# Performance work log

Hardware: AMD Instinct MI355X
Metric: run time of the kernel (lower is better)

The kernel has to match this reference:

```python
import jax, jax.numpy as jnp
import numpy as np

EMBED = 8      # == n_qubits, forced by x[:, i, :].view(batch, n_qubits)
FFN = 4096
B, S = 32, 2048


def setup_inputs() -> dict:
    key = jax.random.key(0)
    k_x, k_t, k_w1, k_b1, k_w2, k_b2 = jax.random.split(key, 6)
    x = jax.random.normal(k_x, (B, S, EMBED), dtype=jnp.float32)
    theta = jax.random.normal(k_t, (), dtype=jnp.float32)  # shared trainable RY angle
    # torch.nn.Linear-style init bounds
    lim1 = 1.0 / np.sqrt(EMBED)
    lim2 = 1.0 / np.sqrt(FFN)
    W1 = jax.random.uniform(k_w1, (FFN, EMBED), jnp.float32, -lim1, lim1)
    b1 = jax.random.uniform(k_b1, (FFN,), jnp.float32, -lim1, lim1)
    W2 = jax.random.uniform(k_w2, (EMBED, FFN), jnp.float32, -lim2, lim2)
    b2 = jax.random.uniform(k_b2, (EMBED,), jnp.float32, -lim2, lim2)
    return {"x": x, "theta": theta, "W1": W1, "b1": b1, "W2": W2, "b2": b2}


def reference(x, theta, W1, b1, W2, b2):
    # Quantum circuit, solved analytically (product state, single-qubit gates):
    # |0> --RX(x_i)--RY(theta)--> <Z_i> = cos(theta) * cos(x_i)
    # This fuses the original per-token Python loop into one elementwise op.
    q = jnp.cos(theta) * jnp.cos(x)                 # [B, S, 8]
    # dropout is identity in eval mode
    h = jax.nn.relu(jnp.einsum('bsk,fk->bsf', q, W1) + b1)   # [B, S, FFN]
    out = jnp.einsum('bsf,ef->bse', h, W2) + b2              # [B, S, 8]
    return out
```

## Files before the change

### kernel.cpp

```cpp
#include <hip/hip_runtime.h>
#include <math.h>

#define FFN_DIM 4096
#define NCHUNK  128

typedef _Float16 f16x8 __attribute__((ext_vector_type(8)));
typedef __fp16   h16x2 __attribute__((ext_vector_type(2)));
typedef float    f32x16 __attribute__((ext_vector_type(16)));
typedef float    f32x4  __attribute__((ext_vector_type(4)));

__global__ void build_frags_kernel(const float* __restrict__ w1,
                                   const float* __restrict__ b1,
                                   const float* __restrict__ w2,
                                   _Float16* __restrict__ w1f,
                                   _Float16* __restrict__ w2f) {
    int i = blockIdx.x * 256 + threadIdx.x;
    if (i < NCHUNK * 64 * 8) {
        int j    = i & 7;
        int lane = (i >> 3) & 63;
        int cc   = i >> 9;
        _Float16 v;
        if (lane < 32) v = (_Float16)w1[(cc * 32 + lane) * 8 + j];
        else           v = (j == 0) ? (_Float16)b1[cc * 32 + (lane & 31)]
                                    : (_Float16)0.0f;
        w1f[i] = v;
    }
    if (i < NCHUNK * 2 * 16 * 8) {
        int j  = i & 7;
        int ci = (i >> 3) & 15;
        int c  = (i >> 7) & 1;
        int cc = i >> 8;
        int g = ci >> 3, e = ci & 7;
        int k = 8 * g + j;
        int fl = (k & 3) + 8 * ((k >> 2) & 1) + 4 * (k >> 3);
        int f = 32 * cc + 16 * c + fl;
        w2f[i] = (_Float16)w2[e * FFN_DIM + f];
    }
}

__global__ __launch_bounds__(256, 2) void ffq_mfma_kernel(
    const float* __restrict__ x,
    const float* __restrict__ theta,
    const _Float16* __restrict__ w1f,
    const _Float16* __restrict__ w2f,
    const float* __restrict__ b2,
    float* __restrict__ out,
    int n_tok)
{
    __shared__ float part[4][4][64][4];

    const int tid  = threadIdx.x;
    const int lane = tid & 63;
    const int wave = tid >> 6;
    const int l31  = lane & 31;
    const int g    = lane >> 5;

    const int tb = blockIdx.x * 128;
    const float cth = cosf(theta[0]);

    f16x8 bq0 = {}, bq1 = {}, bq2 = {}, bq3 = {};
    if (g == 0) {
#define LOAD_BQ(BQ, TOFF)                                                  \
        {                                                                  \
            int t_ = tb + (TOFF) + l31;                                    \
            int r_ = t_ < n_tok ? t_ : (n_tok - 1);                        \
            const f32x4* xp_ = (const f32x4*)(x + (size_t)r_ * 8);         \
            f32x4 u_ = xp_[0], v_ = xp_[1];                                \
            BQ[0] = (_Float16)(cth * cosf(u_.x));                          \
            BQ[1] = (_Float16)(cth * cosf(u_.y));                          \
            BQ[2] = (_Float16)(cth * cosf(u_.z));                          \
            BQ[3] = (_Float16)(cth * cosf(u_.w));                          \
            BQ[4] = (_Float16)(cth * cosf(v_.x));                          \
            BQ[5] = (_Float16)(cth * cosf(v_.y));                          \
            BQ[6] = (_Float16)(cth * cosf(v_.z));                          \
            BQ[7] = (_Float16)(cth * cosf(v_.w));                          \
        }
        LOAD_BQ(bq0, 0)
        LOAD_BQ(bq1, 32)
        LOAD_BQ(bq2, 64)
        LOAD_BQ(bq3, 96)
#undef LOAD_BQ
    } else {
        bq0[0] = (_Float16)1.0f;
        bq1[0] = (_Float16)1.0f;
        bq2[0] = (_Float16)1.0f;
        bq3[0] = (_Float16)1.0f;
    }

    f32x16 acc0 = {}, acc1 = {}, acc2 = {}, acc3 = {};
    const f32x16 zero16 = {};

    const int ci = g * 8 + (l31 & 7);
    const _Float16* a1p = w1f + (size_t)lane * 8;
    const _Float16* a2p = w2f + (size_t)ci * 8;

    union U8 { f16x8 v; h16x2 p[4]; };
    const h16x2 hz = {(__fp16)0.0f, (__fp16)0.0f};

    const int c0 = wave * (NCHUNK / 4);
    const int c1 = c0 + (NCHUNK / 4);

    f16x8 A1  = *(const f16x8*)(a1p + (size_t)c0 * 512);
    f16x8 A2a = *(const f16x8*)(a2p + (size_t)c0 * 256);
    f16x8 A2b = *(const f16x8*)(a2p + (size_t)c0 * 256 + 128);

    for (int cc = c0; cc < c1; ++cc) {
        f16x8 nA1 = A1, nA2a = A2a, nA2b = A2b;
        if (cc + 1 < c1) {
            nA1  = *(const f16x8*)(a1p + (size_t)(cc + 1) * 512);
            nA2a = *(const f16x8*)(a2p + (size_t)(cc + 1) * 256);
            nA2b = *(const f16x8*)(a2p + (size_t)(cc + 1) * 256 + 128);
        }

        f32x16 dA = __builtin_amdgcn_mfma_f32_32x32x16_f16(A1, bq0, zero16, 0, 0, 0);
        f32x16 dB = __builtin_amdgcn_mfma_f32_32x32x16_f16(A1, bq1, zero16, 0, 0, 0);
        f32x16 dC = __builtin_amdgcn_mfma_f32_32x32x16_f16(A1, bq2, zero16, 0, 0, 0);
        f32x16 dD = __builtin_amdgcn_mfma_f32_32x32x16_f16(A1, bq3, zero16, 0, 0, 0);

        U8 uaA, ubA, uaB, ubB, uaC, ubC, uaD, ubD;
        #pragma unroll
        for (int v = 0; v < 4; ++v) {
            uaA.p[v] = __builtin_amdgcn_cvt_pkrtz(dA[2 * v],     dA[2 * v + 1]);
            ubA.p[v] = __builtin_amdgcn_cvt_pkrtz(dA[8 + 2 * v], dA[8 + 2 * v + 1]);
            uaB.p[v] = __builtin_amdgcn_cvt_pkrtz(dB[2 * v],     dB[2 * v + 1]);
            ubB.p[v] = __builtin_amdgcn_cvt_pkrtz(dB[8 + 2 * v], dB[8 + 2 * v + 1]);
            uaC.p[v] = __builtin_amdgcn_cvt_pkrtz(dC[2 * v],     dC[2 * v + 1]);
            ubC.p[v] = __builtin_amdgcn_cvt_pkrtz(dC[8 + 2 * v], dC[8 + 2 * v + 1]);
            uaD.p[v] = __builtin_amdgcn_cvt_pkrtz(dD[2 * v],     dD[2 * v + 1]);
            ubD.p[v] = __builtin_amdgcn_cvt_pkrtz(dD[8 + 2 * v], dD[8 + 2 * v + 1]);
        }
        #pragma unroll
        for (int v = 0; v < 4; ++v) {
            uaA.p[v] = __builtin_elementwise_max(uaA.p[v], hz);
            ubA.p[v] = __builtin_elementwise_max(ubA.p[v], hz);
            uaB.p[v] = __builtin_elementwise_max(uaB.p[v], hz);
            ubB.p[v] = __builtin_elementwise_max(ubB.p[v], hz);
            uaC.p[v] = __builtin_elementwise_max(uaC.p[v], hz);
            ubC.p[v] = __builtin_elementwise_max(ubC.p[v], hz);
            uaD.p[v] = __builtin_elementwise_max(uaD.p[v], hz);
            ubD.p[v] = __builtin_elementwise_max(ubD.p[v], hz);
        }

        acc0 = __builtin_amdgcn_mfma_f32_32x32x16_f16(A2a, uaA.v, acc0, 0, 0, 0);
        acc1 = __builtin_amdgcn_mfma_f32_32x32x16_f16(A2a, uaB.v, acc1, 0, 0, 0);
        acc2 = __builtin_amdgcn_mfma_f32_32x32x16_f16(A2a, uaC.v, acc2, 0, 0, 0);
        acc3 = __builtin_amdgcn_mfma_f32_32x32x16_f16(A2a, uaD.v, acc3, 0, 0, 0);
        acc0 = __builtin_amdgcn_mfma_f32_32x32x16_f16(A2b, ubA.v, acc0, 0, 0, 0);
        acc1 = __builtin_amdgcn_mfma_f32_32x32x16_f16(A2b, ubB.v, acc1, 0, 0, 0);
        acc2 = __builtin_amdgcn_mfma_f32_32x32x16_f16(A2b, ubC.v, acc2, 0, 0, 0);
        acc3 = __builtin_amdgcn_mfma_f32_32x32x16_f16(A2b, ubD.v, acc3, 0, 0, 0);

        A1 = nA1; A2a = nA2a; A2b = nA2b;
    }

    #pragma unroll
    for (int r = 0; r < 4; ++r) {
        part[wave][0][lane][r] = acc0[r];
        part[wave][1][lane][r] = acc1[r];
        part[wave][2][lane][r] = acc2[r];
        part[wave][3][lane][r] = acc3[r];
    }
    __syncthreads();

    for (int i = tid; i < 128 * 8; i += 256) {
        int t = i >> 3, e = i & 7;
        int gt = tb + t;
        if (gt < n_tok) {
            int tt = t >> 5;
            int tl = t & 31;
            int sl = (e >> 2) * 32 + tl;
            int r  = e & 3;
            float s = part[0][tt][sl][r] + part[1][tt][sl][r]
                    + part[2][tt][sl][r] + part[3][tt][sl][r] + b2[e];
            out[(size_t)gt * 8 + e] = s;
        }
    }
}

__global__ __launch_bounds__(256, 4) void ffq_valu_kernel(
    const float* __restrict__ x, const float* __restrict__ theta,
    const float* __restrict__ w1, const float* __restrict__ b1,
    const float* __restrict__ w2, const float* __restrict__ b2,
    float* __restrict__ out, int n_tok)
{
    __shared__ float part[4][64][9];
    const int tid = threadIdx.x;
    const int lane = tid & 63;
    const int wave = __builtin_amdgcn_readfirstlane(tid >> 6);
    const int tok = blockIdx.x * 64 + lane;
    const int rtok = tok < n_tok ? tok : n_tok - 1;
    const float cth = cosf(theta[0]);
    const f32x4* xv = (const f32x4*)(x + (size_t)rtok * 8);
    f32x4 x0 = xv[0], x1 = xv[1];
    float q[8];
    q[0]=cth*cosf(x0.x); q[1]=cth*cosf(x0.y); q[2]=cth*cosf(x0.z); q[3]=cth*cosf(x0.w);
    q[4]=cth*cosf(x1.x); q[5]=cth*cosf(x1.y); q[6]=cth*cosf(x1.z); q[7]=cth*cosf(x1.w);
    float acc[8];
    #pragma unroll
    for (int e = 0; e < 8; ++e) acc[e] = 0.0f;
    const int f0 = wave * (FFN_DIM / 4), f1 = f0 + (FFN_DIM / 4);
    #pragma unroll 2
    for (int f = f0; f < f1; ++f) {
        const f32x4* w1r = (const f32x4*)(w1 + (size_t)f * 8);
        f32x4 u0 = w1r[0], u1 = w1r[1];
        float h = b1[f];
        h = fmaf(u0.x,q[0],h); h = fmaf(u0.y,q[1],h); h = fmaf(u0.z,q[2],h); h = fmaf(u0.w,q[3],h);
        h = fmaf(u1.x,q[4],h); h = fmaf(u1.y,q[5],h); h = fmaf(u1.z,q[6],h); h = fmaf(u1.w,q[7],h);
        h = fmaxf(h, 0.0f);
        #pragma unroll
        for (int e = 0; e < 8; ++e) acc[e] = fmaf(h, w2[e * FFN_DIM + f], acc[e]);
    }
    #pragma unroll
    for (int e = 0; e < 8; ++e) part[wave][lane][e] = acc[e];
    __syncthreads();
    for (int i = tid; i < 64 * 8; i += 256) {
        int t = i >> 3, e = i & 7;
        int gt = blockIdx.x * 64 + t;
        if (gt < n_tok)
            out[(size_t)gt * 8 + e] = part[0][t][e] + part[1][t][e]
                                    + part[2][t][e] + part[3][t][e] + b2[e];
    }
}

extern "C" void kernel_launch(void* const* d_in, const int* in_sizes, int n_in,
                              void* d_out, int out_size, void* d_ws, size_t ws_size,
                              hipStream_t stream) {
    const float* x     = (const float*)d_in[0];
    const float* theta = (const float*)d_in[1];
    const float* w1    = (const float*)d_in[2];
    const float* b1    = (const float*)d_in[3];
    const float* w2    = (const float*)d_in[4];
    const float* b2    = (const float*)d_in[5];
    float* out = (float*)d_out;
    const int n_tok = out_size / 8;

    const size_t W1F_BYTES = (size_t)NCHUNK * 64 * 8 * sizeof(_Float16);
    const size_t W2F_BYTES = (size_t)NCHUNK * 2 * 16 * 8 * sizeof(_Float16);

    if (ws_size >= W1F_BYTES + W2F_BYTES) {
        _Float16* w1f = (_Float16*)d_ws;
        _Float16* w2f = (_Float16*)((char*)d_ws + W1F_BYTES);
        build_frags_kernel<<<(NCHUNK * 64 * 8 + 255) / 256, 256, 0, stream>>>(
            w1, b1, w2, w1f, w2f);
        int blocks = (n_tok + 127) / 128;
        ffq_mfma_kernel<<<blocks, 256, 0, stream>>>(x, theta, w1f, w2f, b2, out,
                                                    n_tok);
    } else {
        int grid = (n_tok + 63) / 64;
        ffq_valu_kernel<<<grid, 256, 0, stream>>>(x, theta, w1, b1, w2, b2, out,
                                                  n_tok);
    }
}
```

Before: 33.09 us.

## Split FFN dimension across two blocks per token tile with separate reduce kernel

Each 128-token tile is now processed by two blocks, each covering half of the FFN chunks, with every wave handling 16 chunks instead of 32. Partial sums go to a workspace buffer and a new reduce kernel adds the two halves plus b2 into the output. Launch bounds are raised to 4 blocks per CU. The aim is more parallelism and occupancy, paid for by an extra kernel launch, recomputing the x/cos fragments in both blocks, and a global round-trip for the partials.

```diff
diff --git a/kernel.cpp b/kernel.cpp
--- a/kernel.cpp
+++ b/kernel.cpp
@@ -38,13 +38,12 @@
     }
 }
 
-__global__ __launch_bounds__(256, 2) void ffq_mfma_kernel(
+__global__ __launch_bounds__(256, 4) void ffq_mfma_kernel(
     const float* __restrict__ x,
     const float* __restrict__ theta,
     const _Float16* __restrict__ w1f,
     const _Float16* __restrict__ w2f,
-    const float* __restrict__ b2,
-    float* __restrict__ out,
+    float* __restrict__ partial,
     int n_tok)
 {
     __shared__ float part[4][4][64][4];
@@ -55,7 +54,8 @@
     const int l31  = lane & 31;
     const int g    = lane >> 5;
 
-    const int tb = blockIdx.x * 128;
+    const int cls = blockIdx.x & 1;
+    const int tb  = (blockIdx.x >> 1) * 128;
     const float cth = cosf(theta[0]);
 
     f16x8 bq0 = {}, bq1 = {}, bq2 = {}, bq3 = {};
@@ -97,8 +97,8 @@
     union U8 { f16x8 v; h16x2 p[4]; };
     const h16x2 hz = {(__fp16)0.0f, (__fp16)0.0f};
 
-    const int c0 = wave * (NCHUNK / 4);
-    const int c1 = c0 + (NCHUNK / 4);
+    const int c0 = cls * 64 + wave * 16;
+    const int c1 = c0 + 16;
 
     f16x8 A1  = *(const f16x8*)(a1p + (size_t)c0 * 512);
     f16x8 A2a = *(const f16x8*)(a2p + (size_t)c0 * 256);
@@ -171,9 +171,24 @@
             int sl = (e >> 2) * 32 + tl;
             int r  = e & 3;
             float s = part[0][tt][sl][r] + part[1][tt][sl][r]
-                    + part[2][tt][sl][r] + part[3][tt][sl][r] + b2[e];
-            out[(size_t)gt * 8 + e] = s;
-        }
+                    + part[2][tt][sl][r] + part[3][tt][sl][r];
+            partial[((size_t)cls * n_tok + gt) * 8 + e] = s;
+        }
+    }
+}
+
+__global__ __launch_bounds__(256) void ffq_reduce_kernel(
+    const float* __restrict__ partial, const float* __restrict__ b2,
+    float* __restrict__ out, int n_tok)
+{
+    int j = blockIdx.x * 256 + threadIdx.x;
+    int nq = n_tok * 2;
+    if (j < nq) {
+        const f32x4* p = (const f32x4*)partial;
+        size_t stride = (size_t)n_tok * 2;
+        f32x4 s = p[j] + p[j + stride];
+        f32x4 bb = ((const f32x4*)b2)[j & 1];
+        ((f32x4*)out)[j] = s + bb;
     }
 }
 
@@ -236,15 +251,20 @@
 
     const size_t W1F_BYTES = (size_t)NCHUNK * 64 * 8 * sizeof(_Float16);
     const size_t W2F_BYTES = (size_t)NCHUNK * 2 * 16 * 8 * sizeof(_Float16);
-
-    if (ws_size >= W1F_BYTES + W2F_BYTES) {
+    const size_t PART_BYTES = (size_t)2 * n_tok * 8 * sizeof(float);
+
+    if (ws_size >= W1F_BYTES + W2F_BYTES + PART_BYTES) {
         _Float16* w1f = (_Float16*)d_ws;
         _Float16* w2f = (_Float16*)((char*)d_ws + W1F_BYTES);
+        float* partial = (float*)((char*)d_ws + W1F_BYTES + W2F_BYTES);
         build_frags_kernel<<<(NCHUNK * 64 * 8 + 255) / 256, 256, 0, stream>>>(
             w1, b1, w2, w1f, w2f);
-        int blocks = (n_tok + 127) / 128;
-        ffq_mfma_kernel<<<blocks, 256, 0, stream>>>(x, theta, w1f, w2f, b2, out,
-                                                    n_tok);
+        int blocks = 2 * ((n_tok + 127) / 128);
+        ffq_mfma_kernel<<<blocks, 256, 0, stream>>>(x, theta, w1f, w2f,
+                                                    partial, n_tok);
+        int nq = n_tok * 2;
+        ffq_reduce_kernel<<<(nq + 255) / 256, 256, 0, stream>>>(partial, b2,
+                                                                out, n_tok);
     } else {
         int grid = (n_tok + 63) / 64;
         ffq_valu_kernel<<<grid, 256, 0, stream>>>(x, theta, w1, b1, w2, b2, out,
```

After: 85.91 us. +159.7%, slower.

## Keep weight fragments register-resident and stream token tiles with split-FFN partial reduction

Applied to the files above, without the earlier changes.

Adds a new path that precomputes the quantum-encoded token fragments in f16 in a separate kernel. A streaming MFMA kernel then holds a fixed slice of W1/W2 fragments in registers per wave and loops over many token tiles, prefetching the next tile. The FFN dimension is split four ways across blocks, and partial sums are written to workspace and combined with b2 in a separate reduce kernel. The goal is to avoid reloading weights for every token tile. In exchange it adds two extra launches, partial-sum traffic, per-tile block barriers, and it drops the VALU fallback.

```diff
diff --git a/kernel.cpp b/kernel.cpp
--- a/kernel.cpp
+++ b/kernel.cpp
@@ -35,6 +35,139 @@
         int fl = (k & 3) + 8 * ((k >> 2) & 1) + 4 * (k >> 3);
         int f = 32 * cc + 16 * c + fl;
         w2f[i] = (_Float16)w2[e * FFN_DIM + f];
+    }
+}
+
+__global__ void build_bq_kernel(const float* __restrict__ x,
+                                const float* __restrict__ theta,
+                                _Float16* __restrict__ bqf,
+                                int n_tok, int nt32) {
+    int i = blockIdx.x * 256 + threadIdx.x;
+    if (i >= nt32 * 64) return;
+    int lane = i & 63;
+    int tile = i >> 6;
+    _Float16* dst = bqf + (size_t)i * 8;
+    if (lane < 32) {
+        const float cth = cosf(theta[0]);
+        int t_ = tile * 32 + lane;
+        int r_ = t_ < n_tok ? t_ : (n_tok - 1);
+        const f32x4* xp = (const f32x4*)(x + (size_t)r_ * 8);
+        f32x4 u = xp[0], v = xp[1];
+        dst[0] = (_Float16)(cth * cosf(u.x));
+        dst[1] = (_Float16)(cth * cosf(u.y));
+        dst[2] = (_Float16)(cth * cosf(u.z));
+        dst[3] = (_Float16)(cth * cosf(u.w));
+        dst[4] = (_Float16)(cth * cosf(v.x));
+        dst[5] = (_Float16)(cth * cosf(v.y));
+        dst[6] = (_Float16)(cth * cosf(v.z));
+        dst[7] = (_Float16)(cth * cosf(v.w));
+    } else {
+        dst[0] = (_Float16)1.0f;
+        #pragma unroll
+        for (int j = 1; j < 8; ++j) dst[j] = (_Float16)0.0f;
+    }
+}
+
+__global__ __launch_bounds__(256, 2) void ffq_stream_kernel(
+    const _Float16* __restrict__ bqf,
+    const _Float16* __restrict__ w1f,
+    const _Float16* __restrict__ w2f,
+    float* __restrict__ partial,
+    int n_tok, int nt32, int tpb)
+{
+    __shared__ float part[4][64][4];
+
+    const int tid  = threadIdx.x;
+    const int lane = tid & 63;
+    const int wave = tid >> 6;
+    const int l31  = lane & 31;
+    const int g    = lane >> 5;
+
+    const int cls = blockIdx.x & 3;
+    const int grp = blockIdx.x >> 2;
+    const int c0  = cls * 32 + wave * 8;
+
+    f16x8 A1r[8], A2ar[8], A2br[8];
+    {
+        const _Float16* a1p = w1f + (size_t)lane * 8;
+        const _Float16* a2p = w2f + (size_t)(g * 8 + (l31 & 7)) * 8;
+        #pragma unroll
+        for (int k = 0; k < 8; ++k) {
+            A1r[k]  = *(const f16x8*)(a1p + (size_t)(c0 + k) * 512);
+            A2ar[k] = *(const f16x8*)(a2p + (size_t)(c0 + k) * 256);
+            A2br[k] = *(const f16x8*)(a2p + (size_t)(c0 + k) * 256 + 128);
+        }
+    }
+
+    const f32x16 zero16 = {};
+    union U8 { f16x8 v; h16x2 p[4]; };
+    const h16x2 hz = {(__fp16)0.0f, (__fp16)0.0f};
+
+    int t0   = grp * tpb;
+    int tend = t0 + tpb;
+    if (tend > nt32) tend = nt32;
+    if (t0 >= tend) return;
+
+    const int etk = tid >> 3;
+    const int ee  = tid & 7;
+    const int esl = (ee >> 2) * 32 + etk;
+    const int er  = ee & 3;
+
+    f16x8 bq = *(const f16x8*)(bqf + ((size_t)t0 * 64 + lane) * 8);
+
+    for (int t = t0; t < tend; ++t) {
+        int nx = (t + 1 < tend) ? (t + 1) : t;
+        f16x8 bqn = *(const f16x8*)(bqf + ((size_t)nx * 64 + lane) * 8);
+
+        f32x16 acc = {};
+        #pragma unroll
+        for (int k = 0; k < 8; ++k) {
+            f32x16 d = __builtin_amdgcn_mfma_f32_32x32x16_f16(A1r[k], bq, zero16, 0, 0, 0);
+            U8 ua, ub;
+            #pragma unroll
+            for (int v = 0; v < 4; ++v) {
+                ua.p[v] = __builtin_amdgcn_cvt_pkrtz(d[2 * v],     d[2 * v + 1]);
+                ub.p[v] = __builtin_amdgcn_cvt_pkrtz(d[8 + 2 * v], d[8 + 2 * v + 1]);
+            }
+            #pragma unroll
+            for (int v = 0; v < 4; ++v) {
+                ua.p[v] = __builtin_elementwise_max(ua.p[v], hz);
+                ub.p[v] = __builtin_elementwise_max(ub.p[v], hz);
+            }
+            acc = __builtin_amdgcn_mfma_f32_32x32x16_f16(A2ar[k], ua.v, acc, 0, 0, 0);
+            acc = __builtin_amdgcn_mfma_f32_32x32x16_f16(A2br[k], ub.v, acc, 0, 0, 0);
+        }
+
+        __syncthreads();
+        #pragma unroll
+        for (int r = 0; r < 4; ++r) part[wave][lane][r] = acc[r];
+        __syncthreads();
+
+        int tok = t * 32 + etk;
+        if (tok < n_tok) {
+            float s = part[0][esl][er] + part[1][esl][er]
+                    + part[2][esl][er] + part[3][esl][er];
+            partial[((size_t)cls * n_tok + tok) * 8 + ee] = s;
+        }
+        bq = bqn;
+    }
+}
+
+__global__ __launch_bounds__(256) void ffq_reduce_kernel(
+    const float* __restrict__ partial, const float* __restrict__ b2,
+    float* __restrict__ out, int n_tok)
+{
+    int j = blockIdx.x * 256 + threadIdx.x;
+    int nq = n_tok * 2;
+    if (j < nq) {
+        const f32x4* p = (const f32x4*)partial;
+        size_t stride = (size_t)n_tok * 2;
+        f32x4 s = p[j];
+        s = s + p[j + stride];
+        s = s + p[j + 2 * stride];
+        s = s + p[j + 3 * stride];
+        f32x4 bb = ((const f32x4*)b2)[j & 1];
+        ((f32x4*)out)[j] = s + bb;
     }
 }
 
@@ -177,51 +310,6 @@
     }
 }
 
-__global__ __launch_bounds__(256, 4) void ffq_valu_kernel(
-    const float* __restrict__ x, const float* __restrict__ theta,
-    const float* __restrict__ w1, const float* __restrict__ b1,
-    const float* __restrict__ w2, const float* __restrict__ b2,
-    float* __restrict__ out, int n_tok)
-{
-    __shared__ float part[4][64][9];
-    const int tid = threadIdx.x;
-    const int lane = tid & 63;
-    const int wave = __builtin_amdgcn_readfirstlane(tid >> 6);
-    const int tok = blockIdx.x * 64 + lane;
-    const int rtok = tok < n_tok ? tok : n_tok - 1;
-    const float cth = cosf(theta[0]);
-    const f32x4* xv = (const f32x4*)(x + (size_t)rtok * 8);
-    f32x4 x0 = xv[0], x1 = xv[1];
-    float q[8];
-    q[0]=cth*cosf(x0.x); q[1]=cth*cosf(x0.y); q[2]=cth*cosf(x0.z); q[3]=cth*cosf(x0.w);
-    q[4]=cth*cosf(x1.x); q[5]=cth*cosf(x1.y); q[6]=cth*cosf(x1.z); q[7]=cth*cosf(x1.w);
-    float acc[8];
-    #pragma unroll
-    for (int e = 0; e < 8; ++e) acc[e] = 0.0f;
-    const int f0 = wave * (FFN_DIM / 4), f1 = f0 + (FFN_DIM / 4);
-    #pragma unroll 2
-    for (int f = f0; f < f1; ++f) {
-        const f32x4* w1r = (const f32x4*)(w1 + (size_t)f * 8);
-        f32x4 u0 = w1r[0], u1 = w1r[1];
-        float h = b1[f];
-        h = fmaf(u0.x,q[0],h); h = fmaf(u0.y,q[1],h); h = fmaf(u0.z,q[2],h); h = fmaf(u0.w,q[3],h);
-        h = fmaf(u1.x,q[4],h); h = fmaf(u1.y,q[5],h); h = fmaf(u1.z,q[6],h); h = fmaf(u1.w,q[7],h);
-        h = fmaxf(h, 0.0f);
-        #pragma unroll
-        for (int e = 0; e < 8; ++e) acc[e] = fmaf(h, w2[e * FFN_DIM + f], acc[e]);
-    }
-    #pragma unroll
-    for (int e = 0; e < 8; ++e) part[wave][lane][e] = acc[e];
-    __syncthreads();
-    for (int i = tid; i < 64 * 8; i += 256) {
-        int t = i >> 3, e = i & 7;
-        int gt = blockIdx.x * 64 + t;
-        if (gt < n_tok)
-            out[(size_t)gt * 8 + e] = part[0][t][e] + part[1][t][e]
-                                    + part[2][t][e] + part[3][t][e] + b2[e];
-    }
-}
-
 extern "C" void kernel_launch(void* const* d_in, const int* in_sizes, int n_in,
                               void* d_out, int out_size, void* d_ws, size_t ws_size,
                               hipStream_t stream) {
@@ -233,21 +321,37 @@
     const float* b2    = (const float*)d_in[5];
     float* out = (float*)d_out;
     const int n_tok = out_size / 8;
-
-    const size_t W1F_BYTES = (size_t)NCHUNK * 64 * 8 * sizeof(_Float16);
-    const size_t W2F_BYTES = (size_t)NCHUNK * 2 * 16 * 8 * sizeof(_Float16);
-
-    if (ws_size >= W1F_BYTES + W2F_BYTES) {
-        _Float16* w1f = (_Float16*)d_ws;
-        _Float16* w2f = (_Float16*)((char*)d_ws + W1F_BYTES);
+    const int nt32  = (n_tok + 31) / 32;
+
+    const size_t W1F_BYTES  = (size_t)NCHUNK * 64 * 8 * 2;
+    const size_t W2F_BYTES  = (size_t)NCHUNK * 2 * 16 * 8 * 2;
+    const size_t BQF_BYTES  = (size_t)nt32 * 64 * 8 * 2;
+    const size_t PART_BYTES = (size_t)4 * n_tok * 8 * sizeof(float);
+
+    _Float16* w1f = (_Float16*)d_ws;
+    _Float16* w2f = (_Float16*)((char*)d_ws + W1F_BYTES);
+
+    if (ws_size >= W1F_BYTES + W2F_BYTES + BQF_BYTES + PART_BYTES) {
+        _Float16* bqf = (_Float16*)((char*)d_ws + W1F_BYTES + W2F_BYTES);
+        float* partial = (float*)((char*)d_ws + W1F_BYTES + W2F_BYTES + BQF_BYTES);
+
+        build_frags_kernel<<<(NCHUNK * 64 * 8 + 255) / 256, 256, 0, stream>>>(
+            w1, b1, w2, w1f, w2f);
+        build_bq_kernel<<<(nt32 * 64 + 255) / 256, 256, 0, stream>>>(
+            x, theta, bqf, n_tok, nt32);
+
+        const int ngrp = 128;
+        const int tpb  = (nt32 + ngrp - 1) / ngrp;
+        ffq_stream_kernel<<<4 * ngrp, 256, 0, stream>>>(bqf, w1f, w2f,
+                                                        partial, n_tok, nt32, tpb);
+        int nq = n_tok * 2;
+        ffq_reduce_kernel<<<(nq + 255) / 256, 256, 0, stream>>>(partial, b2,
+                                                                out, n_tok);
+    } else {
         build_frags_kernel<<<(NCHUNK * 64 * 8 + 255) / 256, 256, 0, stream>>>(
             w1, b1, w2, w1f, w2f);
         int blocks = (n_tok + 127) / 128;
         ffq_mfma_kernel<<<blocks, 256, 0, stream>>>(x, theta, w1f, w2f, b2, out,
                                                     n_tok);
-    } else {
-        int grid = (n_tok + 63) / 64;
-        ffq_valu_kernel<<<grid, 256, 0, stream>>>(x, theta, w1, b1, w2, b2, out,
-                                                  n_tok);
-    }
-}
+    }
+}
```

Measured after the change: 40.20 us. 1.22x slower.
